# Optimization experiments

Measured on AMD Instinct MI355X. Metric: run time of the kernel, lower is better.

## Reference

```python
import jax, jax.numpy as jnp
import numpy as np

D_MODEL = 1024
D_STATE = 16
D_CONV = 4
EXPAND = 2
D_INNER = EXPAND * D_MODEL          # 2048
DT_RANK = (D_MODEL + 15) // 16      # ceil(d_model/16) = 64
BATCH = 2
SEQ_LEN = 2048


def setup_inputs() -> dict:
    key = jax.random.key(0)
    ks = jax.random.split(key, 8)
    s = 0.02
    x = jax.random.normal(ks[0], (BATCH, SEQ_LEN, D_MODEL), dtype=jnp.float32)
    in_proj_w = jax.random.normal(ks[1], (2 * D_INNER, D_MODEL), dtype=jnp.float32) * s
    conv_w = jax.random.normal(ks[2], (D_INNER, 1, D_CONV), dtype=jnp.float32) * s  # depthwise (O,I/g,K)
    conv_b = jax.random.normal(ks[3], (D_INNER,), dtype=jnp.float32) * s
    x_proj_w = jax.random.normal(ks[4], (DT_RANK + 2 * D_STATE, D_INNER), dtype=jnp.float32) * s
    dt_proj_w = jax.random.normal(ks[5], (D_INNER, DT_RANK), dtype=jnp.float32) * s
    dt_proj_b = jax.random.normal(ks[6], (D_INNER,), dtype=jnp.float32) * s
    A_log = jnp.log(jnp.tile(jnp.arange(1, D_STATE + 1, dtype=jnp.float32), (D_INNER, 1)))
    D = jnp.ones((D_INNER,), dtype=jnp.float32)
    out_proj_w = jax.random.normal(ks[7], (D_MODEL, D_INNER), dtype=jnp.float32) * s
    return {"x": x, "in_proj_w": in_proj_w, "conv_w": conv_w, "conv_b": conv_b,
            "x_proj_w": x_proj_w, "dt_proj_w": dt_proj_w, "dt_proj_b": dt_proj_b,
            "A_log": A_log, "D": D, "out_proj_w": out_proj_w}


def reference(x, in_proj_w, conv_w, conv_b, x_proj_w, dt_proj_w, dt_proj_b, A_log, D, out_proj_w):
    Bsz, L, _ = x.shape
    d_inner = D.shape[0]
    d_state = A_log.shape[1]
    dt_rank = dt_proj_w.shape[1]

    # input projection -> (B, L, 2*d_inner), split into ssm branch and gate branch
    x_and_res = x @ in_proj_w.T
    xs, res = jnp.split(x_and_res, 2, axis=-1)

    # causal depthwise conv1d: pad left by d_conv-1 (torch pads both sides then slices [:L])
    xc = jnp.swapaxes(xs, 1, 2)  # (B, d_inner, L)
    xc = jax.lax.conv_general_dilated(
        xc, conv_w, window_strides=(1,), padding=[(conv_w.shape[-1] - 1, 0)],
        dimension_numbers=("NCH", "OIH", "NCH"), feature_group_count=d_inner)
    xc = xc + conv_b[None, :, None]
    u = jax.nn.silu(jnp.swapaxes(xc, 1, 2))  # (B, L, d_inner)

    # data-dependent SSM parameters
    x_dbl = u @ x_proj_w.T  # (B, L, dt_rank + 2*d_state)
    dt_r = x_dbl[..., :dt_rank]
    B_ssm = x_dbl[..., dt_rank:dt_rank + d_state]
    C_ssm = x_dbl[..., dt_rank + d_state:]
    dt = dt_r @ dt_proj_w.T + dt_proj_b
    dt = jnp.minimum(jax.nn.softplus(dt), 10.0)  # softplus then clamp(max=10)

    A = -jnp.exp(A_log)  # (d_inner, d_state)

    def step(h, inp):
        dt_t, B_t, C_t, u_t = inp  # (B,di), (B,ds), (B,ds), (B,di)
        dA = jnp.exp(dt_t[:, :, None] * A)               # (B, di, ds)
        h = dA * h + (dt_t * u_t)[:, :, None] * B_t[:, None, :]
        y_t = jnp.einsum("bds,bs->bd", h, C_t) + D * u_t
        return h, y_t

    h0 = jnp.zeros((Bsz, d_inner, d_state), dtype=x.dtype)
    xs_t = (jnp.swapaxes(dt, 0, 1), jnp.swapaxes(B_ssm, 0, 1),
            jnp.swapaxes(C_ssm, 0, 1), jnp.swapaxes(u, 0, 1))
    _, ys = jax.lax.scan(step, h0, xs_t)  # ys: (L, B, d_inner)
    y = jnp.swapaxes(ys, 0, 1)

    y = y * jax.nn.silu(res)
    return y @ out_proj_w.T
```

## Files before the change

### kernel.cpp

```cpp
#include <hip/hip_runtime.h>
#include <hip/hip_bf16.h>
#include <stdint.h>

#define BATCH 2
#define SEQLEN 2048
#define DMODEL 1024
#define DINNER 2048
#define DSTATE 16
#define DTRANK 64
#define NPROJ 128
#define NROWS (BATCH*SEQLEN)
#define NCHUNK 64
#define TCC 32
#define LOG2E 1.4426950408889634f

typedef __bf16 bf16;
typedef __bf16 bf16x8 __attribute__((ext_vector_type(8)));
typedef __bf16 bf16x4 __attribute__((ext_vector_type(4)));
typedef float  floatx4 __attribute__((ext_vector_type(4)));

#if __has_builtin(__builtin_amdgcn_exp2f)
#define EXP2F __builtin_amdgcn_exp2f
#else
#define EXP2F exp2f
#endif

__device__ __forceinline__ float sigmoidf_(float x) { return 1.f / (1.f + __expf(-x)); }
__device__ __forceinline__ float siluf_(float x)    { return x * sigmoidf_(x); }

__device__ __forceinline__ void gload_lds16(const void* gsrc, void* ldsdst) {
  auto g = (const __attribute__((address_space(1))) uint32_t*)(uintptr_t)gsrc;
  uint32_t lo = (uint32_t)(uintptr_t)ldsdst;
  auto l = (__attribute__((address_space(3))) uint32_t*)lo;
  __builtin_amdgcn_global_load_lds(g, l, 16, 0, 0);
}

#define CAST_XN   (NROWS * DMODEL)
#define CAST_WIN  (2 * DINNER * DMODEL)
#define CAST_WON  (DMODEL * DINNER)
#define CAST_XWN  (NPROJ * DINNER)
#define CAST_TOT4 ((CAST_XN + CAST_WIN + CAST_WON + CAST_XWN) / 4)

__device__ __forceinline__ void cvt4(const float* in, bf16* out) {
  floatx4 v = *(const floatx4*)in;
  bf16x4 o;
  #pragma unroll
  for (int j = 0; j < 4; ++j) o[j] = (bf16)v[j];
  *(bf16x4*)out = o;
}

__global__ __launch_bounds__(256) void cast_all_k(const float* __restrict__ x,
                                                  const float* __restrict__ wi,
                                                  const float* __restrict__ wo,
                                                  const float* __restrict__ xw,
                                                  bf16* __restrict__ x_bf,
                                                  bf16* __restrict__ wi_bf,
                                                  bf16* __restrict__ wo_bf,
                                                  bf16* __restrict__ xw_bf) {
  const int i = blockIdx.x * 256 + threadIdx.x;
  const int e = i * 4;
  if (e < CAST_XN) {
    cvt4(x + e, x_bf + e);
  } else if (e < CAST_XN + CAST_WIN) {
    const int o = e - CAST_XN;
    cvt4(wi + o, wi_bf + o);
  } else if (e < CAST_XN + CAST_WIN + CAST_WON) {
    const int o = e - CAST_XN - CAST_WIN;
    cvt4(wo + o, wo_bf + o);
  } else {
    const int o = e - CAST_XN - CAST_WIN - CAST_WON;
    const int row = o >> 11;
    bf16x4 z;
    if (row < 96) {
      cvt4(xw + o, xw_bf + o);
    } else {
      #pragma unroll
      for (int j = 0; j < 4; ++j) z[j] = (bf16)0.f;
      *(bf16x4*)&xw_bf[o] = z;
    }
  }
}

__global__ __launch_bounds__(512, 2) void gemm_bt_256(const bf16* __restrict__ A,
                                                      const bf16* __restrict__ Bm,
                                                      bf16* __restrict__ C,
                                                      int M, int N, int K) {
  __shared__ bf16 As[4][256][32];
  __shared__ bf16 Bs[4][256][32];
  const int tid  = threadIdx.x;
  const int lane = tid & 63;
  const int wave = tid >> 6;
  const int wm = wave >> 2;
  const int wn = wave & 3;
  const int fr = lane & 15;
  const int fq = lane >> 4;
  const int bm = blockIdx.y * 256;
  const int bn = blockIdx.x * 256;
  const int NT = K >> 5;

  const int arow = tid >> 2;
  const int slot = tid & 3;
  const int scol = ((slot ^ (arow & 3)) << 3);
  const bf16* gA0 = A  + (size_t)(bm + arow) * K + scol;
  const bf16* gA1 = A  + (size_t)(bm + 128 + arow) * K + scol;
  const bf16* gB0 = Bm + (size_t)(bn + arow) * K + scol;
  const bf16* gB1 = Bm + (size_t)(bn + 128 + arow) * K + scol;
  char* lA0 = (char*)As + arow * 64 + slot * 16;
  char* lB0 = (char*)Bs + arow * 64 + slot * 16;

#define STAGE256(kt) do {                                   \
    const int bi_ = (kt) & 3;                               \
    const size_t ko_ = (size_t)(kt) << 5;                   \
    gload_lds16(gA0 + ko_, lA0 + bi_ * 16384);              \
    gload_lds16(gA1 + ko_, lA0 + 8192 + bi_ * 16384);       \
    gload_lds16(gB0 + ko_, lB0 + bi_ * 16384);              \
    gload_lds16(gB1 + ko_, lB0 + 8192 + bi_ * 16384);       \
  } while (0)

  const int aoff = ((fq ^ (fr & 3)) << 4);
  const char* rA = (char*)As + aoff + (wm * 128 + fr) * 64;
  const char* rB = (char*)Bs + aoff + (wn * 64 + fr) * 64;

  floatx4 acc[8][4];
  #pragma unroll
  for (int m = 0; m < 8; ++m)
    #pragma unroll
    for (int n = 0; n < 4; ++n)
      #pragma unroll
      for (int r = 0; r < 4; ++r) acc[m][n][r] = 0.f;

  STAGE256(0);
  STAGE256(1);
  STAGE256(2);
  __builtin_amdgcn_sched_barrier(0);
  asm volatile("s_waitcnt vmcnt(8)" ::: "memory");
  __builtin_amdgcn_s_barrier();
  __builtin_amdgcn_sched_barrier(0);

  for (int kt = 0; kt < NT; ++kt) {
    const int bi = kt & 3;
    if (kt + 3 < NT) STAGE256(kt + 3);
    const char* pa = rA + bi * 16384;
    const char* pb = rB + bi * 16384;
    bf16x8 a8[8], b8[4];
    #pragma unroll
    for (int m = 0; m < 8; ++m) a8[m] = *(const bf16x8*)(pa + m * 1024);
    #pragma unroll
    for (int n = 0; n < 4; ++n) b8[n] = *(const bf16x8*)(pb + n * 1024);
    __builtin_amdgcn_s_setprio(1);
    #pragma unroll
    for (int m = 0; m < 8; ++m)
      #pragma unroll
      for (int n = 0; n < 4; ++n)
        acc[m][n] = __builtin_amdgcn_mfma_f32_16x16x32_bf16(a8[m], b8[n], acc[m][n], 0, 0, 0);
    __builtin_amdgcn_s_setprio(0);
    if (kt < NT - 1) {
      __builtin_amdgcn_sched_barrier(0);
      if (kt <= NT - 4)      { asm volatile("s_waitcnt vmcnt(8)" ::: "memory"); }
      else if (kt == NT - 3) { asm volatile("s_waitcnt vmcnt(4)" ::: "memory"); }
      else                   { asm volatile("s_waitcnt vmcnt(0)" ::: "memory"); }
      __builtin_amdgcn_s_barrier();
      __builtin_amdgcn_sched_barrier(0);
    }
  }
#undef STAGE256

  #pragma unroll
  for (int m = 0; m < 8; ++m) {
    const int row = bm + wm * 128 + (m << 4) + (fq << 2);
    #pragma unroll
    for (int n = 0; n < 4; ++n) {
      const int col = bn + wn * 64 + (n << 4) + fr;
      #pragma unroll
      for (int r = 0; r < 4; ++r)
        C[(size_t)(row + r) * N + col] = (bf16)acc[m][n][r];
    }
  }
}

__global__ __launch_bounds__(256) void gemm_bt_sk(const bf16* __restrict__ A,
                                                  const bf16* __restrict__ Bm,
                                                  float* __restrict__ Cp,
                                                  int M, int N, int ldk, int KS) {
  __shared__ bf16 As[128 * 32];
  __shared__ bf16 Bs[128 * 32];
  const int tid  = threadIdx.x;
  const int lane = tid & 63;
  const int wave = tid >> 6;
  const int bm = blockIdx.y * 128;
  const int bn = blockIdx.x * 128;
  const int z  = blockIdx.z;
  const int wr = (wave >> 1) << 6;
  const int wc = (wave & 1) << 6;
  const int fr = lane & 15;
  const int fq = lane >> 4;

  const int srow  = tid >> 2;
  const int skoff = (tid & 3) << 3;
  const size_t kbase = (size_t)z * KS + skoff;
  const bf16* ga0 = A  + (size_t)(bm + srow) * ldk + kbase;
  const bf16* ga1 = A  + (size_t)(bm + 64 + srow) * ldk + kbase;
  const bf16* gb0 = Bm + (size_t)(bn + srow) * ldk + kbase;
  const bf16* gb1 = Bm + (size_t)(bn + 64 + srow) * ldk + kbase;
  char* la0 = (char*)As + (wave << 10);
  char* la1 = (char*)As + 4096 + (wave << 10);
  char* lb0 = (char*)Bs + (wave << 10);
  char* lb1 = (char*)Bs + 4096 + (wave << 10);

  floatx4 acc[4][4];
  #pragma unroll
  for (int i = 0; i < 4; ++i)
    #pragma unroll
    for (int j = 0; j < 4; ++j)
      #pragma unroll
      for (int r = 0; r < 4; ++r) acc[i][j][r] = 0.f;

  for (int k0 = 0; k0 < KS; k0 += 32) {
    gload_lds16(ga0 + k0, la0);
    gload_lds16(ga1 + k0, la1);
    gload_lds16(gb0 + k0, lb0);
    gload_lds16(gb1 + k0, lb1);
    __syncthreads();
    bf16x8 af[4], bfr[4];
    #pragma unroll
    for (int i = 0; i < 4; ++i)
      af[i] = *(const bf16x8*)&As[(wr + (i << 4) + fr) * 32 + (fq << 3)];
    #pragma unroll
    for (int j = 0; j < 4; ++j)
      bfr[j] = *(const bf16x8*)&Bs[(wc + (j << 4) + fr) * 32 + (fq << 3)];
    #pragma unroll
    for (int i = 0; i < 4; ++i)
      #pragma unroll
      for (int j = 0; j < 4; ++j)
        acc[i][j] = __builtin_amdgcn_mfma_f32_16x16x32_bf16(af[i], bfr[j], acc[i][j], 0, 0, 0);
    __syncthreads();
  }
  float* Cb = Cp + (size_t)z * M * N;
  #pragma unroll
  for (int i = 0; i < 4; ++i) {
    const int row = bm + wr + (i << 4) + (fq << 2);
    #pragma unroll
    for (int j = 0; j < 4; ++j) {
      const int col = bn + wc + (j << 4) + fr;
      #pragma unroll
      for (int r = 0; r < 4; ++r)
        Cb[(size_t)(row + r) * N + col] = acc[i][j][r];
    }
  }
}

template <int KS>
__global__ __launch_bounds__(256) void reduce_sk_k(const float* __restrict__ part,
                                                   float* __restrict__ out,
                                                   int n4, size_t mn) {
  const int i = blockIdx.x * 256 + threadIdx.x;
  if (i >= n4) return;
  const size_t e = (size_t)i * 4;
  floatx4 s = *(const floatx4*)&part[e];
  #pragma unroll
  for (int z = 1; z < KS; ++z) {
    floatx4 v = *(const floatx4*)&part[(size_t)z * mn + e];
    #pragma unroll
    for (int j = 0; j < 4; ++j) s[j] += v[j];
  }
  *(floatx4*)&out[e] = s;
}

__global__ __launch_bounds__(256) void conv_silu_k(const bf16* __restrict__ xr,
                                                   const float* __restrict__ cw,
                                                   const float* __restrict__ cb,
                                                   bf16* __restrict__ u_btd,
                                                   bf16* __restrict__ u_dtl) {
  __shared__ float tile[32][65];
  const int tid = threadIdx.x;
  const int d0 = blockIdx.x << 6;
  const int t0 = blockIdx.y << 5;
  const int b  = blockIdx.z;
  const int dl = tid & 63, tq = tid >> 6;
  const int d  = d0 + dl;
  const float w0 = cw[d * 4 + 0], w1 = cw[d * 4 + 1], w2 = cw[d * 4 + 2], w3 = cw[d * 4 + 3];
  const float bias = cb[d];
  #pragma unroll
  for (int i = 0; i < 8; ++i) {
    const int t = tq * 8 + i;
    const int tg = t0 + t;
    float acc = bias;
    {
      int tt = tg - 3;
      if (tt >= 0) acc += w0 * (float)xr[((size_t)b * SEQLEN + tt) * 4096 + d];
    }
    {
      int tt = tg - 2;
      if (tt >= 0) acc += w1 * (float)xr[((size_t)b * SEQLEN + tt) * 4096 + d];
    }
    {
      int tt = tg - 1;
      if (tt >= 0) acc += w2 * (float)xr[((size_t)b * SEQLEN + tt) * 4096 + d];
    }
    acc += w3 * (float)xr[((size_t)b * SEQLEN + tg) * 4096 + d];
    const float uval = siluf_(acc);
    u_btd[((size_t)b * SEQLEN + tg) * DINNER + d] = (bf16)uval;
    tile[t][dl] = uval;
  }
  __syncthreads();
  const int dr = tid >> 2;
  const int tcol = (tid & 3) << 3;
  bf16x8 ov;
  #pragma unroll
  for (int i = 0; i < 8; ++i) ov[i] = (bf16)tile[tcol + i][dr];
  *(bf16x8*)&u_dtl[((size_t)b * DINNER + d0 + dr) * SEQLEN + t0 + tcol] = ov;
}

__global__ __launch_bounds__(256) void dtproj_k(const float* __restrict__ x_dbl,
                                                const float* __restrict__ w,
                                                const float* __restrict__ bias,
                                                bf16* __restrict__ dt_t) {
  __shared__ float r_s[64][65];
  __shared__ float w_s[64][65];
  const int tid  = threadIdx.x;
  const int d0   = blockIdx.x << 6;
  const int row0 = blockIdx.y << 6;
  #pragma unroll
  for (int j = 0; j < 4; ++j) {
    int id = tid + (j << 8);
    int r  = id >> 4;
    int kq = (id & 15) << 2;
    floatx4 v = *(const floatx4*)&x_dbl[(size_t)(row0 + r) * NPROJ + kq];
    r_s[r][kq] = v[0]; r_s[r][kq + 1] = v[1]; r_s[r][kq + 2] = v[2]; r_s[r][kq + 3] = v[3];
    floatx4 ww = *(const floatx4*)&w[(size_t)(d0 + r) * 64 + kq];
    w_s[r][kq] = ww[0]; w_s[r][kq + 1] = ww[1]; w_s[r][kq + 2] = ww[2]; w_s[r][kq + 3] = ww[3];
  }
  __syncthreads();
  const int tl = tid & 15, dl = tid >> 4;
  float acc[4][4] = {};
  #pragma unroll 8
  for (int k = 0; k < 64; ++k) {
    float a[4], bb[4];
    #pragma unroll
    for (int i = 0; i < 4; ++i) a[i] = r_s[tl * 4 + i][k];
    #pragma unroll
    for (int j = 0; j < 4; ++j) bb[j] = w_s[dl + (j << 4)][k];
    #pragma unroll
    for (int i = 0; i < 4; ++i)
      #pragma unroll
      for (int j = 0; j < 4; ++j) acc[i][j] += a[i] * bb[j];
  }
  const int bb_ = row0 >> 11;
  const int tbase = (row0 & 2047) + tl * 4;
  #pragma unroll
  for (int j = 0; j < 4; ++j) {
    const int dd = d0 + dl + (j << 4);
    const float bsv = bias[dd];
    bf16x4 o;
    #pragma unroll
    for (int i = 0; i < 4; ++i) {
      float v = acc[i][j] + bsv;
      float sp = (v > 20.f) ? v : __logf(1.f + __expf(v));
      o[i] = (bf16)fminf(sp, 10.f);
    }
    *(bf16x4*)&dt_t[((size_t)bb_ * DINNER + dd) * SEQLEN + tbase] = o;
  }
}

__global__ __launch_bounds__(256) void scanA_k(const bf16* __restrict__ dt_t,
                                               const bf16* __restrict__ u_dtl,
                                               const float* __restrict__ x_dbl,
                                               const float* __restrict__ A_log,
                                               float* __restrict__ hfin,
                                               float* __restrict__ Pbuf) {
  __shared__ float Bs_[TCC][16];
  const int tid = threadIdx.x;
  const int b = blockIdx.z, c = blockIdx.y;
  const int d = (blockIdx.x << 8) + tid;
  const int t0 = c * TCC;
  if (tid < TCC * 4) {
    const int t = tid >> 2, sq = (tid & 3) << 2;
    *(floatx4*)&Bs_[t][sq] = *(const floatx4*)&x_dbl[((size_t)b * SEQLEN + t0 + t) * NPROJ + 64 + sq];
  }
  float Ae[DSTATE];
  #pragma unroll
  for (int q = 0; q < 4; ++q) {
    floatx4 al = *(const floatx4*)&A_log[d * DSTATE + q * 4];
    #pragma unroll
    for (int j = 0; j < 4; ++j) Ae[q * 4 + j] = -__expf(al[j]) * LOG2E;
  }
  __syncthreads();
  float h[DSTATE];
  #pragma unroll
  for (int s = 0; s < DSTATE; ++s) h[s] = 0.f;
  float sdt = 0.f;
  const bf16* dtp = dt_t + ((size_t)b * DINNER + d) * SEQLEN + t0;
  const bf16* up  = u_dtl + ((size_t)b * DINNER + d) * SEQLEN + t0;
  for (int tq = 0; tq < TCC; tq += 8) {
    bf16x8 dt8 = *(const bf16x8*)&dtp[tq];
    bf16x8 u8  = *(const bf16x8*)&up[tq];
    #pragma unroll
    for (int j = 0; j < 8; ++j) {
      const float dtv = (float)dt8[j];
      const float xin = dtv * (float)u8[j];
      sdt += dtv;
      floatx4 Brow[4];
      #pragma unroll
      for (int q = 0; q < 4; ++q) Brow[q] = *(const floatx4*)&Bs_[tq + j][q * 4];
      #pragma unroll
      for (int s = 0; s < DSTATE; ++s)
        h[s] = EXP2F(dtv * Ae[s]) * h[s] + xin * Brow[s >> 2][s & 3];
    }
  }
  const size_t base = (((size_t)b * NCHUNK + c) * DINNER + d) * DSTATE;
  #pragma unroll
  for (int q = 0; q < 4; ++q) {
    floatx4 hv, pv;
    #pragma unroll
    for (int j = 0; j < 4; ++j) {
      hv[j] = h[q * 4 + j];
      pv[j] = EXP2F(Ae[q * 4 + j] * sdt);
    }
    *(floatx4*)&hfin[base + q * 4] = hv;
    *(floatx4*)&Pbuf[base + q * 4] = pv;
  }
}

__global__ __launch_bounds__(256) void scanB_k(const float* __restrict__ hfin,
                                               const float* __restrict__ Pbuf,
                                               float* __restrict__ hin) {
  const int flat = blockIdx.x * 256 + threadIdx.x;
  const int b  = flat >> 15;
  const int ds = flat & 32767;
  float h = 0.f;
  hin[((size_t)b * NCHUNK) * 32768 + ds] = 0.f;
  for (int c = 1; c < NCHUNK; ++c) {
    const size_t prev = ((size_t)(b * NCHUNK + c - 1)) * 32768 + ds;
    h = hfin[prev] + Pbuf[prev] * h;
    hin[((size_t)(b * NCHUNK + c)) * 32768 + ds] = h;
  }
}

__global__ __launch_bounds__(256) void scanC_k(const bf16* __restrict__ dt_t,
                                               const bf16* __restrict__ u_dtl,
                                               const float* __restrict__ x_dbl,
                                               const float* __restrict__ A_log,
                                               const float* __restrict__ Dp,
                                               const float* __restrict__ hin,
                                               const bf16* __restrict__ xr,
                                               bf16* __restrict__ yres) {
  __shared__ float Bs_[TCC][16];
  __shared__ float Cs_[TCC][16];
  const int tid = threadIdx.x;
  const int b = blockIdx.z, c = blockIdx.y;
  const int d = (blockIdx.x << 8) + tid;
  const int t0 = c * TCC;
  if (tid < TCC * 4) {
    const int t = tid >> 2, sq = (tid & 3) << 2;
    *(floatx4*)&Bs_[t][sq] = *(const floatx4*)&x_dbl[((size_t)b * SEQLEN + t0 + t) * NPROJ + 64 + sq];
    *(floatx4*)&Cs_[t][sq] = *(const floatx4*)&x_dbl[((size_t)b * SEQLEN + t0 + t) * NPROJ + 80 + sq];
  }
  float Ae[DSTATE];
  #pragma unroll
  for (int q = 0; q < 4; ++q) {
    floatx4 al = *(const floatx4*)&A_log[d * DSTATE + q * 4];
    #pragma unroll
    for (int j = 0; j < 4; ++j) Ae[q * 4 + j] = -__expf(al[j]) * LOG2E;
  }
  float h[DSTATE];
  const size_t base = (((size_t)b * NCHUNK + c) * DINNER + d) * DSTATE;
  #pragma unroll
  for (int q = 0; q < 4; ++q) {
    floatx4 hv = *(const floatx4*)&hin[base + q * 4];
    #pragma unroll
    for (int j = 0; j < 4; ++j) h[q * 4 + j] = hv[j];
  }
  const float Dv = Dp[d];
  __syncthreads();
  const bf16* dtp = dt_t + ((size_t)b * DINNER + d) * SEQLEN + t0;
  const bf16* up  = u_dtl + ((size_t)b * DINNER + d) * SEQLEN + t0;
  const bf16* resp = xr + ((size_t)b * SEQLEN + t0) * 4096 + 2048 + d;
  bf16* yp = yres + ((size_t)b * SEQLEN + t0) * DINNER + d;
  for (int tq = 0; tq < TCC; tq += 8) {
    bf16x8 dt8 = *(const bf16x8*)&dtp[tq];
    bf16x8 u8  = *(const bf16x8*)&up[tq];
    #pragma unroll
    for (int j = 0; j < 8; ++j) {
      const int t = tq + j;
      const float dtv = (float)dt8[j];
      const float uv  = (float)u8[j];
      const float xin = dtv * uv;
      floatx4 Brow[4], Crow[4];
      #pragma unroll
      for (int q = 0; q < 4; ++q) {
        Brow[q] = *(const floatx4*)&Bs_[t][q * 4];
        Crow[q] = *(const floatx4*)&Cs_[t][q * 4];
      }
      float a4[4];
      #pragma unroll
      for (int q = 0; q < 4; ++q) a4[q] = 0.f;
      #pragma unroll
      for (int s = 0; s < DSTATE; ++s) {
        h[s] = EXP2F(dtv * Ae[s]) * h[s] + xin * Brow[s >> 2][s & 3];
        a4[s & 3] += h[s] * Crow[s >> 2][s & 3];
      }
      const float acc = ((a4[0] + a4[1]) + (a4[2] + a4[3])) + Dv * uv;
      const float r = (float)resp[(size_t)t * 4096];
      yp[(size_t)t * DINNER] = (bf16)(acc * siluf_(r));
    }
  }
}

extern "C" void kernel_launch(void* const* d_in, const int* in_sizes, int n_in,
                              void* d_out, int out_size, void* d_ws, size_t ws_size,
                              hipStream_t stream) {
  const float* x         = (const float*)d_in[0];
  const float* in_proj_w = (const float*)d_in[1];
  const float* conv_w    = (const float*)d_in[2];
  const float* conv_b    = (const float*)d_in[3];
  const float* x_proj_w  = (const float*)d_in[4];
  const float* dt_proj_w = (const float*)d_in[5];
  const float* dt_proj_b = (const float*)d_in[6];
  const float* A_log     = (const float*)d_in[7];
  const float* Dp        = (const float*)d_in[8];
  const float* out_proj_w= (const float*)d_in[9];
  float* out = (float*)d_out;

  char* ws = (char*)d_ws;
  size_t off = 0;
  auto alloc = [&](size_t bytes) -> void* {
    void* p = ws + off;
    off += (bytes + 255) & ~(size_t)255;
    return p;
  };
  bf16*  wo_bf  = (bf16*) alloc((size_t)DMODEL * DINNER * 2);
  bf16*  xw_bf  = (bf16*) alloc((size_t)NPROJ * DINNER * 2);
  bf16*  yres   = (bf16*) alloc((size_t)NROWS * DINNER * 2);
  float* x_dbl  = (float*)alloc((size_t)NROWS * NPROJ * 4);
  bf16*  dt_t   = (bf16*) alloc((size_t)BATCH * DINNER * SEQLEN * 2);
  bf16*  u_dtl  = (bf16*) alloc((size_t)BATCH * DINNER * SEQLEN * 2);
  float* hfin   = (float*)alloc((size_t)BATCH * NCHUNK * DINNER * DSTATE * 4);
  float* Pbuf   = (float*)alloc((size_t)BATCH * NCHUNK * DINNER * DSTATE * 4);
  float* hin    = (float*)alloc((size_t)BATCH * NCHUNK * DINNER * DSTATE * 4);
  const size_t mark = off;
  bf16*  x_bf   = (bf16*) alloc((size_t)NROWS * DMODEL * 2);
  bf16*  wi_bf  = (bf16*) alloc((size_t)2 * DINNER * DMODEL * 2);
  bf16*  xr     = (bf16*) alloc((size_t)NROWS * 4096 * 2);
  bf16*  u_btd  = (bf16*) alloc((size_t)NROWS * DINNER * 2);
  float* xpart  = (float*)(ws + mark);
  float* opart  = (float*)(ws + mark);

  cast_all_k<<<CAST_TOT4 / 256, 256, 0, stream>>>(x, in_proj_w, out_proj_w, x_proj_w,
                                                  x_bf, wi_bf, wo_bf, xw_bf);
  gemm_bt_256<<<dim3(4096 / 256, NROWS / 256), 512, 0, stream>>>(x_bf, wi_bf, xr, NROWS, 4096, DMODEL);
  conv_silu_k<<<dim3(DINNER / 64, SEQLEN / 32, BATCH), 256, 0, stream>>>(xr, conv_w, conv_b, u_btd, u_dtl);
  gemm_bt_sk<<<dim3(1, 32, 8), 256, 0, stream>>>(u_btd, xw_bf, xpart, NROWS, NPROJ, DINNER, DINNER / 8);
  reduce_sk_k<8><<<(NROWS * NPROJ / 4 + 255) / 256, 256, 0, stream>>>(xpart, x_dbl, NROWS * NPROJ / 4, (size_t)NROWS * NPROJ);
  dtproj_k<<<dim3(DINNER / 64, NROWS / 64), 256, 0, stream>>>(x_dbl, dt_proj_w, dt_proj_b, dt_t);
  scanA_k<<<dim3(DINNER / 256, NCHUNK, BATCH), 256, 0, stream>>>(dt_t, u_dtl, x_dbl, A_log, hfin, Pbuf);
  scanB_k<<<dim3(BATCH * DINNER * DSTATE / 256), 256, 0, stream>>>(hfin, Pbuf, hin);
  scanC_k<<<dim3(DINNER / 256, NCHUNK, BATCH), 256, 0, stream>>>(dt_t, u_dtl, x_dbl, A_log, Dp, hin, xr, yres);
  gemm_bt_sk<<<dim3(DMODEL / 128, NROWS / 128, 4), 256, 0, stream>>>(yres, wo_bf, opart, NROWS, DMODEL, DINNER, DINNER / 4);
  reduce_sk_k<4><<<(NROWS * DMODEL / 4 + 255) / 256, 256, 0, stream>>>(opart, out, NROWS * DMODEL / 4, (size_t)NROWS * DMODEL);
}
```

Before: 243.5 us.

## Split scan states across half-waves, widen LDS swizzle, store out-proj partials in bf16

Three separate changes. The scan kernels now give each d channel two threads that each hold 8 of the 16 states, joined by a cross-lane shuffle, which doubles the thread count and halves per-thread register pressure and serial work. The 256-tile GEMM's LDS swizzle gains an extra XOR term to cut bank conflicts. The output-projection split-K partials are written as bf16 instead of fp32, halving partial traffic but losing precision in the final sum.

```diff
diff --git a/kernel.cpp b/kernel.cpp
--- a/kernel.cpp
+++ b/kernel.cpp
@@ -100,7 +100,7 @@
 
   const int arow = tid >> 2;
   const int slot = tid & 3;
-  const int scol = ((slot ^ (arow & 3)) << 3);
+  const int scol = ((slot ^ (arow & 3) ^ ((arow >> 2) & 3)) << 3);
   const bf16* gA0 = A  + (size_t)(bm + arow) * K + scol;
   const bf16* gA1 = A  + (size_t)(bm + 128 + arow) * K + scol;
   const bf16* gB0 = Bm + (size_t)(bn + arow) * K + scol;
@@ -117,7 +117,7 @@
     gload_lds16(gB1 + ko_, lB0 + 8192 + bi_ * 16384);       \
   } while (0)
 
-  const int aoff = ((fq ^ (fr & 3)) << 4);
+  const int aoff = ((fq ^ (fr & 3) ^ ((fr >> 2) & 3)) << 4);
   const char* rA = (char*)As + aoff + (wm * 128 + fr) * 64;
   const char* rB = (char*)Bs + aoff + (wn * 64 + fr) * 64;
 
@@ -178,9 +178,10 @@
   }
 }
 
+template <typename PT>
 __global__ __launch_bounds__(256) void gemm_bt_sk(const bf16* __restrict__ A,
                                                   const bf16* __restrict__ Bm,
-                                                  float* __restrict__ Cp,
+                                                  PT* __restrict__ Cp,
                                                   int M, int N, int ldk, int KS) {
   __shared__ bf16 As[128 * 32];
   __shared__ bf16 Bs[128 * 32];
@@ -235,7 +236,7 @@
         acc[i][j] = __builtin_amdgcn_mfma_f32_16x16x32_bf16(af[i], bfr[j], acc[i][j], 0, 0, 0);
     __syncthreads();
   }
-  float* Cb = Cp + (size_t)z * M * N;
+  PT* Cb = Cp + (size_t)z * M * N;
   #pragma unroll
   for (int i = 0; i < 4; ++i) {
     const int row = bm + wr + (i << 4) + (fq << 2);
@@ -244,24 +245,24 @@
       const int col = bn + wc + (j << 4) + fr;
       #pragma unroll
       for (int r = 0; r < 4; ++r)
-        Cb[(size_t)(row + r) * N + col] = acc[i][j][r];
-    }
-  }
-}
-
-template <int KS>
-__global__ __launch_bounds__(256) void reduce_sk_k(const float* __restrict__ part,
+        Cb[(size_t)(row + r) * N + col] = (PT)acc[i][j][r];
+    }
+  }
+}
+
+template <int KS, typename PT>
+__global__ __launch_bounds__(256) void reduce_sk_k(const PT* __restrict__ part,
                                                    float* __restrict__ out,
                                                    int n4, size_t mn) {
   const int i = blockIdx.x * 256 + threadIdx.x;
   if (i >= n4) return;
   const size_t e = (size_t)i * 4;
-  floatx4 s = *(const floatx4*)&part[e];
-  #pragma unroll
-  for (int z = 1; z < KS; ++z) {
-    floatx4 v = *(const floatx4*)&part[(size_t)z * mn + e];
-    #pragma unroll
-    for (int j = 0; j < 4; ++j) s[j] += v[j];
+  floatx4 s = {0.f, 0.f, 0.f, 0.f};
+  #pragma unroll
+  for (int z = 0; z < KS; ++z) {
+    const PT* p = &part[(size_t)z * mn + e];
+    #pragma unroll
+    for (int j = 0; j < 4; ++j) s[j] += (float)p[j];
   }
   *(floatx4*)&out[e] = s;
 }
@@ -371,23 +372,27 @@
   __shared__ float Bs_[TCC][16];
   const int tid = threadIdx.x;
   const int b = blockIdx.z, c = blockIdx.y;
-  const int d = (blockIdx.x << 8) + tid;
+  const int wave = tid >> 6, lane = tid & 63;
+  const int sh = lane >> 5;
+  const int dl = (wave << 5) + (lane & 31);
+  const int d  = (blockIdx.x << 7) + dl;
   const int t0 = c * TCC;
   if (tid < TCC * 4) {
     const int t = tid >> 2, sq = (tid & 3) << 2;
     *(floatx4*)&Bs_[t][sq] = *(const floatx4*)&x_dbl[((size_t)b * SEQLEN + t0 + t) * NPROJ + 64 + sq];
   }
-  float Ae[DSTATE];
-  #pragma unroll
-  for (int q = 0; q < 4; ++q) {
-    floatx4 al = *(const floatx4*)&A_log[d * DSTATE + q * 4];
-    #pragma unroll
-    for (int j = 0; j < 4; ++j) Ae[q * 4 + j] = -__expf(al[j]) * LOG2E;
+  const int s0 = sh << 3;
+  float Ae[8];
+  {
+    floatx4 a0 = *(const floatx4*)&A_log[d * DSTATE + s0];
+    floatx4 a1 = *(const floatx4*)&A_log[d * DSTATE + s0 + 4];
+    #pragma unroll
+    for (int j = 0; j < 4; ++j) { Ae[j] = -__expf(a0[j]) * LOG2E; Ae[4 + j] = -__expf(a1[j]) * LOG2E; }
   }
   __syncthreads();
-  float h[DSTATE];
-  #pragma unroll
-  for (int s = 0; s < DSTATE; ++s) h[s] = 0.f;
+  float h[8];
+  #pragma unroll
+  for (int s = 0; s < 8; ++s) h[s] = 0.f;
   float sdt = 0.f;
   const bf16* dtp = dt_t + ((size_t)b * DINNER + d) * SEQLEN + t0;
   const bf16* up  = u_dtl + ((size_t)b * DINNER + d) * SEQLEN + t0;
@@ -399,26 +404,24 @@
       const float dtv = (float)dt8[j];
       const float xin = dtv * (float)u8[j];
       sdt += dtv;
-      floatx4 Brow[4];
-      #pragma unroll
-      for (int q = 0; q < 4; ++q) Brow[q] = *(const floatx4*)&Bs_[tq + j][q * 4];
-      #pragma unroll
-      for (int s = 0; s < DSTATE; ++s)
-        h[s] = EXP2F(dtv * Ae[s]) * h[s] + xin * Brow[s >> 2][s & 3];
-    }
-  }
-  const size_t base = (((size_t)b * NCHUNK + c) * DINNER + d) * DSTATE;
-  #pragma unroll
-  for (int q = 0; q < 4; ++q) {
-    floatx4 hv, pv;
-    #pragma unroll
-    for (int j = 0; j < 4; ++j) {
-      hv[j] = h[q * 4 + j];
-      pv[j] = EXP2F(Ae[q * 4 + j] * sdt);
-    }
-    *(floatx4*)&hfin[base + q * 4] = hv;
-    *(floatx4*)&Pbuf[base + q * 4] = pv;
-  }
+      const floatx4 B0 = *(const floatx4*)&Bs_[tq + j][s0];
+      const floatx4 B1 = *(const floatx4*)&Bs_[tq + j][s0 + 4];
+      #pragma unroll
+      for (int s = 0; s < 4; ++s) {
+        h[s]     = EXP2F(dtv * Ae[s]) * h[s]     + xin * B0[s];
+        h[4 + s] = EXP2F(dtv * Ae[4 + s]) * h[4 + s] + xin * B1[s];
+      }
+    }
+  }
+  const size_t base = (((size_t)b * NCHUNK + c) * DINNER + d) * DSTATE + s0;
+  floatx4 hv0, hv1, pv0, pv1;
+  #pragma unroll
+  for (int j = 0; j < 4; ++j) {
+    hv0[j] = h[j];     pv0[j] = EXP2F(Ae[j] * sdt);
+    hv1[j] = h[4 + j]; pv1[j] = EXP2F(Ae[4 + j] * sdt);
+  }
+  *(floatx4*)&hfin[base] = hv0;     *(floatx4*)&hfin[base + 4] = hv1;
+  *(floatx4*)&Pbuf[base] = pv0;     *(floatx4*)&Pbuf[base + 4] = pv1;
 }
 
 __global__ __launch_bounds__(256) void scanB_k(const float* __restrict__ hfin,
@@ -448,27 +451,31 @@
   __shared__ float Cs_[TCC][16];
   const int tid = threadIdx.x;
   const int b = blockIdx.z, c = blockIdx.y;
-  const int d = (blockIdx.x << 8) + tid;
+  const int wave = tid >> 6, lane = tid & 63;
+  const int sh = lane >> 5;
+  const int dl = (wave << 5) + (lane & 31);
+  const int d  = (blockIdx.x << 7) + dl;
   const int t0 = c * TCC;
   if (tid < TCC * 4) {
     const int t = tid >> 2, sq = (tid & 3) << 2;
     *(floatx4*)&Bs_[t][sq] = *(const floatx4*)&x_dbl[((size_t)b * SEQLEN + t0 + t) * NPROJ + 64 + sq];
     *(floatx4*)&Cs_[t][sq] = *(const floatx4*)&x_dbl[((size_t)b * SEQLEN + t0 + t) * NPROJ + 80 + sq];
   }
-  float Ae[DSTATE];
-  #pragma unroll
-  for (int q = 0; q < 4; ++q) {
-    floatx4 al = *(const floatx4*)&A_log[d * DSTATE + q * 4];
-    #pragma unroll
-    for (int j = 0; j < 4; ++j) Ae[q * 4 + j] = -__expf(al[j]) * LOG2E;
-  }
-  float h[DSTATE];
-  const size_t base = (((size_t)b * NCHUNK + c) * DINNER + d) * DSTATE;
-  #pragma unroll
-  for (int q = 0; q < 4; ++q) {
-    floatx4 hv = *(const floatx4*)&hin[base + q * 4];
-    #pragma unroll
-    for (int j = 0; j < 4; ++j) h[q * 4 + j] = hv[j];
+  const int s0 = sh << 3;
+  float Ae[8];
+  {
+    floatx4 a0 = *(const floatx4*)&A_log[d * DSTATE + s0];
+    floatx4 a1 = *(const floatx4*)&A_log[d * DSTATE + s0 + 4];
+    #pragma unroll
+    for (int j = 0; j < 4; ++j) { Ae[j] = -__expf(a0[j]) * LOG2E; Ae[4 + j] = -__expf(a1[j]) * LOG2E; }
+  }
+  float h[8];
+  const size_t base = (((size_t)b * NCHUNK + c) * DINNER + d) * DSTATE + s0;
+  {
+    floatx4 h0 = *(const floatx4*)&hin[base];
+    floatx4 h1 = *(const floatx4*)&hin[base + 4];
+    #pragma unroll
+    for (int j = 0; j < 4; ++j) { h[j] = h0[j]; h[4 + j] = h1[j]; }
   }
   const float Dv = Dp[d];
   __syncthreads();
@@ -485,23 +492,24 @@
       const float dtv = (float)dt8[j];
       const float uv  = (float)u8[j];
       const float xin = dtv * uv;
-      floatx4 Brow[4], Crow[4];
-      #pragma unroll
-      for (int q = 0; q < 4; ++q) {
-        Brow[q] = *(const floatx4*)&Bs_[t][q * 4];
-        Crow[q] = *(const floatx4*)&Cs_[t][q * 4];
+      const floatx4 B0 = *(const floatx4*)&Bs_[t][s0];
+      const floatx4 B1 = *(const floatx4*)&Bs_[t][s0 + 4];
+      const floatx4 C0 = *(const floatx4*)&Cs_[t][s0];
+      const floatx4 C1 = *(const floatx4*)&Cs_[t][s0 + 4];
+      float a0 = 0.f, a1 = 0.f;
+      #pragma unroll
+      for (int s = 0; s < 4; ++s) {
+        h[s]     = EXP2F(dtv * Ae[s]) * h[s]     + xin * B0[s];
+        h[4 + s] = EXP2F(dtv * Ae[4 + s]) * h[4 + s] + xin * B1[s];
+        a0 += h[s] * C0[s];
+        a1 += h[4 + s] * C1[s];
       }
-      float a4[4];
-      #pragma unroll
-      for (int q = 0; q < 4; ++q) a4[q] = 0.f;
-      #pragma unroll
-      for (int s = 0; s < DSTATE; ++s) {
-        h[s] = EXP2F(dtv * Ae[s]) * h[s] + xin * Brow[s >> 2][s & 3];
-        a4[s & 3] += h[s] * Crow[s >> 2][s & 3];
+      float acc = a0 + a1;
+      acc += __shfl_xor(acc, 32);
+      if (sh == 0) {
+        const float r = (float)resp[(size_t)t * 4096];
+        yp[(size_t)t * DINNER] = (bf16)((acc + Dv * uv) * siluf_(r));
       }
-      const float acc = ((a4[0] + a4[1]) + (a4[2] + a4[3])) + Dv * uv;
-      const float r = (float)resp[(size_t)t * 4096];
-      yp[(size_t)t * DINNER] = (bf16)(acc * siluf_(r));
     }
   }
 }
@@ -543,18 +551,18 @@
   bf16*  xr     = (bf16*) alloc((size_t)NROWS * 4096 * 2);
   bf16*  u_btd  = (bf16*) alloc((size_t)NROWS * DINNER * 2);
   float* xpart  = (float*)(ws + mark);
-  float* opart  = (float*)(ws + mark);
+  bf16*  opart  = (bf16*)(ws + mark);
 
   cast_all_k<<<CAST_TOT4 / 256, 256, 0, stream>>>(x, in_proj_w, out_proj_w, x_proj_w,
                                                   x_bf, wi_bf, wo_bf, xw_bf);
   gemm_bt_256<<<dim3(4096 / 256, NROWS / 256), 512, 0, stream>>>(x_bf, wi_bf, xr, NROWS, 4096, DMODEL);
   conv_silu_k<<<dim3(DINNER / 64, SEQLEN / 32, BATCH), 256, 0, stream>>>(xr, conv_w, conv_b, u_btd, u_dtl);
-  gemm_bt_sk<<<dim3(1, 32, 8), 256, 0, stream>>>(u_btd, xw_bf, xpart, NROWS, NPROJ, DINNER, DINNER / 8);
-  reduce_sk_k<8><<<(NROWS * NPROJ / 4 + 255) / 256, 256, 0, stream>>>(xpart, x_dbl, NROWS * NPROJ / 4, (size_t)NROWS * NPROJ);
+  gemm_bt_sk<float><<<dim3(1, 32, 8), 256, 0, stream>>>(u_btd, xw_bf, xpart, NROWS, NPROJ, DINNER, DINNER / 8);
+  reduce_sk_k<8, float><<<(NROWS * NPROJ / 4 + 255) / 256, 256, 0, stream>>>(xpart, x_dbl, NROWS * NPROJ / 4, (size_t)NROWS * NPROJ);
   dtproj_k<<<dim3(DINNER / 64, NROWS / 64), 256, 0, stream>>>(x_dbl, dt_proj_w, dt_proj_b, dt_t);
-  scanA_k<<<dim3(DINNER / 256, NCHUNK, BATCH), 256, 0, stream>>>(dt_t, u_dtl, x_dbl, A_log, hfin, Pbuf);
+  scanA_k<<<dim3(DINNER / 128, NCHUNK, BATCH), 256, 0, stream>>>(dt_t, u_dtl, x_dbl, A_log, hfin, Pbuf);
   scanB_k<<<dim3(BATCH * DINNER * DSTATE / 256), 256, 0, stream>>>(hfin, Pbuf, hin);
-  scanC_k<<<dim3(DINNER / 256, NCHUNK, BATCH), 256, 0, stream>>>(dt_t, u_dtl, x_dbl, A_log, Dp, hin, xr, yres);
-  gemm_bt_sk<<<dim3(DMODEL / 128, NROWS / 128, 4), 256, 0, stream>>>(yres, wo_bf, opart, NROWS, DMODEL, DINNER, DINNER / 4);
-  reduce_sk_k<4><<<(NROWS * DMODEL / 4 + 255) / 256, 256, 0, stream>>>(opart, out, NROWS * DMODEL / 4, (size_t)NROWS * DMODEL);
-}
+  scanC_k<<<dim3(DINNER / 128, NCHUNK, BATCH), 256, 0, stream>>>(dt_t, u_dtl, x_dbl, A_log, Dp, hin, xr, yres);
+  gemm_bt_sk<bf16><<<dim3(DMODEL / 128, NROWS / 128, 4), 256, 0, stream>>>(yres, wo_bf, opart, NROWS, DMODEL, DINNER, DINNER / 4);
+  reduce_sk_k<4, bf16><<<(NROWS * DMODEL / 4 + 255) / 256, 256, 0, stream>>>(opart, out, NROWS * DMODEL / 4, (size_t)NROWS * DMODEL);
+}
```

Result: no change. 242.2 us (-0.5%).
